# Performance work log

Hardware: AMD Instinct MI355X
Metric: run time of the kernel (lower is better)

The kernel has to match this reference:

```python
import jax, jax.numpy as jnp
import numpy as np

K_STEPS = 12
NUM_NEG = 10
B, C, T = 2, 512, 4096


def setup_inputs() -> dict:
    key = jax.random.key(0)
    k0, k1, k2, k3, k4 = jax.random.split(key, 5)
    feat_enc = jax.random.normal(k0, (B, C, T), dtype=jnp.float32)
    feat_context = jax.random.normal(k1, (B, C, T), dtype=jnp.float32)
    W = jax.random.normal(k2, (C, C), dtype=jnp.float32) / np.float32(np.sqrt(C))
    b = jax.random.normal(k3, (C,), dtype=jnp.float32) * 0.01
    # stands in for torch.multinomial draws inside the k-loop: one [T, num_neg]
    # index set per step (values in [0, T))
    neg_idx = jax.random.randint(k4, (K_STEPS, T, NUM_NEG), 0, T, dtype=jnp.int32)
    return {"feat_enc": feat_enc, "feat_context": feat_context, "W": W, "b": b,
            "neg_idx": neg_idx}


def reference(feat_enc, feat_context, W, b, neg_idx):
    # linear over channel dim: (transpose -> Linear -> transpose) == einsum
    c = jnp.einsum('bct,dc->bdt', feat_context, W) + b[None, :, None]  # [B,C,T]
    # cont[b,t,s] = sum_c z[b,c,t] * c[b,c,s]  -> [B,T,T]
    cont = jnp.einsum('bct,bcs->bts', feat_enc, c)
    Bn, Tlen, _ = cont.shape
    total = jnp.zeros((), dtype=cont.dtype)
    for k in range(K_STEPS):
        # positives: diagonal offset=-k -> cont[b, i+k, i], length T-k
        pos = jnp.diagonal(cont, offset=-k, axis1=1, axis2=2)
        pos_loss = jnp.sum(jax.nn.log_sigmoid(pos))
        # torch: neg[b, s, r] = cont[b, s, neg_idx[k, r, s]] for s<num_neg
        idx = neg_idx[k].T  # [num_neg, T]
        idx_b = jnp.broadcast_to(idx[None], (Bn, NUM_NEG, Tlen))
        neg = jnp.take_along_axis(cont[:, :NUM_NEG, :], idx_b, axis=2)
        neg_loss = jnp.sum(jax.nn.log_sigmoid(-neg))
        total = total + pos_loss + NUM_NEG * neg_loss
    return total
```

## Files before the change

### kernel.cpp

```cpp
#include <hip/hip_runtime.h>
#include <hip/hip_bf16.h>

constexpr int KST  = 12;
constexpr int NN   = 10;
constexpr int B    = 2;
constexpr int C    = 512;
constexpr int T    = 4096;
constexpr int BAND = 12;

typedef float f32x4  __attribute__((ext_vector_type(4)));
typedef short bf16x8 __attribute__((ext_vector_type(8)));

__device__ __forceinline__ float logsig(float x) {
    return fminf(x, 0.0f) - log1pf(expf(-fabsf(x)));
}
__device__ __forceinline__ unsigned short f2bf(float f) {
    union { float f; unsigned u; } v; v.f = f;
    unsigned r = v.u + 0x7fff + ((v.u >> 16) & 1);
    return (unsigned short)(r >> 16);
}

__global__ __launch_bounds__(256) void cast_w(
    const float* __restrict__ W, unsigned short* __restrict__ Wh)
{
    const int i = (blockIdx.x * 256 + threadIdx.x) * 4;
    const float4 v = *(const float4*)&W[i];
    short4 o;
    o.x = (short)f2bf(v.x);
    o.y = (short)f2bf(v.y);
    o.z = (short)f2bf(v.z);
    o.w = (short)f2bf(v.w);
    *(short4*)&Wh[i] = o;
}

__global__ __launch_bounds__(512) void fused_kernel(
    const unsigned short* __restrict__ Wh, const float* __restrict__ FC,
    const float* __restrict__ enc, const float* __restrict__ bias,
    float* __restrict__ negls, float* __restrict__ out)
{
    const int b  = blockIdx.y;
    const int n0 = blockIdx.x * 32;

    __shared__ unsigned short Bs[2][32][40];
    __shared__ unsigned short c_t[32 * 512];
    __shared__ unsigned short A_t[64 * 512];
    __shared__ float posred[8];

    const int tid  = threadIdx.x;
    const int lane = tid & 63;
    const int w    = tid >> 6;
    const int l15  = lane & 15;
    const int l4   = lane >> 4;
    const int mw   = w * 64;

    const int skk = tid >> 4;
    const int snn = (tid & 15) * 2;

    const float* FCb  = FC  + (size_t)b * C * T;
    const float* encb = enc + (size_t)b * C * T;

    f32x4 acc[4][2] = {};
    const unsigned short* Abase = Wh + (size_t)(mw + l15) * C + 8 * l4;

    float2 v = *(const float2*)&FCb[(size_t)skk * T + n0 + snn];
    bf16x8 afr[4];
    #pragma unroll
    for (int i = 0; i < 4; ++i) afr[i] = *(const bf16x8*)(Abase + i * 16 * C);

    Bs[0][snn][skk]     = f2bf(v.x);
    Bs[0][snn + 1][skk] = f2bf(v.y);

    int cur = 0;
    for (int ks = 0; ks < 16; ++ks) {
        __syncthreads();
        const int kn = (ks < 15) ? ks + 1 : 15;
        float2 vn = *(const float2*)&FCb[(size_t)(kn * 32 + skk) * T + n0 + snn];
        bf16x8 afn[4];
        #pragma unroll
        for (int i = 0; i < 4; ++i)
            afn[i] = *(const bf16x8*)(Abase + i * 16 * C + kn * 32);

        const bf16x8 bfr0 = *(const bf16x8*)&Bs[cur][l15][8 * l4];
        const bf16x8 bfr1 = *(const bf16x8*)&Bs[cur][16 + l15][8 * l4];

        #pragma unroll
        for (int i = 0; i < 4; ++i) {
            acc[i][0] = __builtin_amdgcn_mfma_f32_16x16x32_bf16(afr[i], bfr0, acc[i][0], 0, 0, 0);
            acc[i][1] = __builtin_amdgcn_mfma_f32_16x16x32_bf16(afr[i], bfr1, acc[i][1], 0, 0, 0);
        }
        Bs[cur ^ 1][snn][skk]     = f2bf(vn.x);
        Bs[cur ^ 1][snn + 1][skk] = f2bf(vn.y);
        #pragma unroll
        for (int i = 0; i < 4; ++i) afr[i] = afn[i];
        cur ^= 1;
    }

    #pragma unroll
    for (int i = 0; i < 4; ++i) {
        const int mb = mw + i * 16 + l4 * 4;
        const float4 bv = *(const float4*)&bias[mb];
        const int g = mb >> 3;
        #pragma unroll
        for (int j = 0; j < 2; ++j) {
            const int sp = j * 16 + l15;
            ushort4 u;
            u.x = f2bf(acc[i][j][0] + bv.x);
            u.y = f2bf(acc[i][j][1] + bv.y);
            u.z = f2bf(acc[i][j][2] + bv.z);
            u.w = f2bf(acc[i][j][3] + bv.w);
            const int off = sp * 1024 + ((g ^ (sp & 7)) << 4) + ((mb & 4) << 1);
            *(ushort4*)((char*)c_t + off) = u;
        }
    }

    {
        const bool safe = (n0 + 48 <= T);
        const int rr    = tid >> 3;
        const int cbase = (tid & 7) * 8;
        for (int dd = 0; dd < 8; ++dd) {
            const int d = dd * 64 + rr;
            float vals[8];
            if (cbase < 48) {
                if (safe) {
                    const float* p = encb + (size_t)d * T + n0 + cbase;
                    *(float4*)&vals[0] = *(const float4*)p;
                    *(float4*)&vals[4] = *(const float4*)(p + 4);
                } else {
                    #pragma unroll
                    for (int e = 0; e < 8; ++e) {
                        int t = n0 + cbase + e;
                        t = t < T ? t : T - 1;
                        vals[e] = encb[(size_t)d * T + t];
                    }
                }
            } else {
                const float* p = encb + (size_t)d * T + (cbase - 48);
                *(float4*)&vals[0] = *(const float4*)p;
                *(float4*)&vals[4] = *(const float4*)(p + 4);
            }
            const int gd = d >> 3;
            const int dl = (d & 7) << 1;
            #pragma unroll
            for (int e = 0; e < 8; ++e) {
                const int c = cbase + e;
                const int off = c * 1024 + ((gd ^ e) << 4) + dl;
                *(unsigned short*)((char*)A_t + off) = f2bf(vals[e]);
            }
        }
    }
    __syncthreads();

    const int i2 = w >> 1;
    const int j2 = w & 1;
    const int rg = i2 * 16 + l15;
    const int ci = (rg < 44) ? rg : ((rg < 54) ? rg + 4 : 63);
    const int sr = j2 * 16 + l15;
    const char* Abyte = (const char*)A_t + ci * 1024;
    const char* Bbyte = (const char*)c_t + sr * 1024;
    const int ax = ci & 7, bx = sr & 7;

    f32x4 dacc = {};
    #pragma unroll
    for (int ks = 0; ks < 16; ++ks) {
        const int ga = ks * 4 + l4;
        const bf16x8 a2 = *(const bf16x8*)(Abyte + ((ga ^ ax) << 4));
        const bf16x8 b2 = *(const bf16x8*)(Bbyte + ((ga ^ bx) << 4));
        dacc = __builtin_amdgcn_mfma_f32_16x16x32_bf16(a2, b2, dacc, 0, 0, 0);
    }

    float pos = 0.0f;
    const int colr = j2 * 16 + l15;
    const int scol = n0 + colr;
    #pragma unroll
    for (int r = 0; r < 4; ++r) {
        const int row = i2 * 16 + l4 * 4 + r;
        const float vv = dacc[r];
        if (row < 44) {
            const int k = row - colr;
            if (k >= 0 && k < BAND && scol + k < T) pos += logsig(vv);
        } else if (row < 54) {
            negls[((size_t)b * NN + (row - 44)) * T + scol] = logsig(-vv);
        }
    }
    #pragma unroll
    for (int off = 32; off > 0; off >>= 1) pos += __shfl_down(pos, off, 64);
    if (lane == 0) posred[w] = pos;
    __syncthreads();
    if (tid == 0) {
        float tsum = 0.0f;
        #pragma unroll
        for (int q = 0; q < 8; ++q) tsum += posred[q];
        atomicAdd(out, tsum);
    }
}

__global__ __launch_bounds__(256) void gather_kernel(
    const int4* __restrict__ nidx4, const float* __restrict__ negls,
    float* __restrict__ out)
{
    const int i4 = blockIdx.x * 256 + threadIdx.x;
    const int4 vv = nidx4[i4];
    const int base = i4 * 4;
    const int idxs[4] = {vv.x, vv.y, vv.z, vv.w};
    float local = 0.0f;
    #pragma unroll
    for (int e = 0; e < 4; ++e) {
        const int n = (base + e) % NN;
        local += negls[(size_t)n * T + idxs[e]]
               + negls[(size_t)(NN + n) * T + idxs[e]];
    }
    #pragma unroll
    for (int off = 32; off > 0; off >>= 1) local += __shfl_down(local, off, 64);
    __shared__ float wsum[4];
    if ((threadIdx.x & 63) == 0) wsum[threadIdx.x >> 6] = local;
    __syncthreads();
    if (threadIdx.x == 0)
        atomicAdd(out, (float)NN * (wsum[0] + wsum[1] + wsum[2] + wsum[3]));
}

extern "C" void kernel_launch(void* const* d_in, const int* in_sizes, int n_in,
                              void* d_out, int out_size, void* d_ws, size_t ws_size,
                              hipStream_t stream)
{
    const float* enc  = (const float*)d_in[0];
    const float* fc   = (const float*)d_in[1];
    const float* W    = (const float*)d_in[2];
    const float* bias = (const float*)d_in[3];
    const int*   nidx = (const int*)d_in[4];
    float* out = (float*)d_out;

    unsigned short* Wh = (unsigned short*)d_ws;
    float* negls = (float*)((char*)d_ws + (size_t)C * C * sizeof(unsigned short));

    hipMemsetAsync(out, 0, sizeof(float), stream);

    cast_w<<<C * C / (256 * 4), 256, 0, stream>>>(W, Wh);
    fused_kernel<<<dim3(T / 32, B), 512, 0, stream>>>(Wh, fc, enc, bias, negls, out);
    gather_kernel<<<KST * T * NN / (4 * 256), 256, 0, stream>>>(
        (const int4*)nidx, negls, out);
}
```

Baseline: 57.30 us.

## Stage full FC tile in LDS once, drop per-step syncs in projection GEMM

Replaces the double-buffered 32x32 FC staging loop (16 iterations each with a __syncthreads) with one up-front load in which each thread reads a full 32-wide row of FC and writes a swizzled bf16 tile covering all 512 channels. The projection GEMM then runs from LDS with no barriers in the K loop, and the result c is written back into the same LDS buffer, so the separate c_t array is removed. This is meant to cut barrier and latency overhead and to overlap the FC loads with the enc loads. In exchange, each thread issues wide loads of 32 floats, which raises register pressure, and the LDS stores use a scattered 2-byte pattern.

```diff
diff --git a/kernel.cpp b/kernel.cpp
--- a/kernel.cpp
+++ b/kernel.cpp
@@ -41,8 +41,7 @@
     const int b  = blockIdx.y;
     const int n0 = blockIdx.x * 32;
 
-    __shared__ unsigned short Bs[2][32][40];
-    __shared__ unsigned short c_t[32 * 512];
+    __shared__ unsigned short fc_t[32 * 512];
     __shared__ unsigned short A_t[64 * 512];
     __shared__ float posred[8];
 
@@ -53,63 +52,22 @@
     const int l4   = lane >> 4;
     const int mw   = w * 64;
 
-    const int skk = tid >> 4;
-    const int snn = (tid & 15) * 2;
-
     const float* FCb  = FC  + (size_t)b * C * T;
     const float* encb = enc + (size_t)b * C * T;
 
-    f32x4 acc[4][2] = {};
-    const unsigned short* Abase = Wh + (size_t)(mw + l15) * C + 8 * l4;
-
-    float2 v = *(const float2*)&FCb[(size_t)skk * T + n0 + snn];
-    bf16x8 afr[4];
-    #pragma unroll
-    for (int i = 0; i < 4; ++i) afr[i] = *(const bf16x8*)(Abase + i * 16 * C);
-
-    Bs[0][snn][skk]     = f2bf(v.x);
-    Bs[0][snn + 1][skk] = f2bf(v.y);
-
-    int cur = 0;
-    for (int ks = 0; ks < 16; ++ks) {
-        __syncthreads();
-        const int kn = (ks < 15) ? ks + 1 : 15;
-        float2 vn = *(const float2*)&FCb[(size_t)(kn * 32 + skk) * T + n0 + snn];
-        bf16x8 afn[4];
-        #pragma unroll
-        for (int i = 0; i < 4; ++i)
-            afn[i] = *(const bf16x8*)(Abase + i * 16 * C + kn * 32);
-
-        const bf16x8 bfr0 = *(const bf16x8*)&Bs[cur][l15][8 * l4];
-        const bf16x8 bfr1 = *(const bf16x8*)&Bs[cur][16 + l15][8 * l4];
-
-        #pragma unroll
-        for (int i = 0; i < 4; ++i) {
-            acc[i][0] = __builtin_amdgcn_mfma_f32_16x16x32_bf16(afr[i], bfr0, acc[i][0], 0, 0, 0);
-            acc[i][1] = __builtin_amdgcn_mfma_f32_16x16x32_bf16(afr[i], bfr1, acc[i][1], 0, 0, 0);
-        }
-        Bs[cur ^ 1][snn][skk]     = f2bf(vn.x);
-        Bs[cur ^ 1][snn + 1][skk] = f2bf(vn.y);
-        #pragma unroll
-        for (int i = 0; i < 4; ++i) afr[i] = afn[i];
-        cur ^= 1;
-    }
-
-    #pragma unroll
-    for (int i = 0; i < 4; ++i) {
-        const int mb = mw + i * 16 + l4 * 4;
-        const float4 bv = *(const float4*)&bias[mb];
-        const int g = mb >> 3;
-        #pragma unroll
-        for (int j = 0; j < 2; ++j) {
-            const int sp = j * 16 + l15;
-            ushort4 u;
-            u.x = f2bf(acc[i][j][0] + bv.x);
-            u.y = f2bf(acc[i][j][1] + bv.y);
-            u.z = f2bf(acc[i][j][2] + bv.z);
-            u.w = f2bf(acc[i][j][3] + bv.w);
-            const int off = sp * 1024 + ((g ^ (sp & 7)) << 4) + ((mb & 4) << 1);
-            *(ushort4*)((char*)c_t + off) = u;
+    {
+        const int k = tid;
+        const float* p = FCb + (size_t)k * T + n0;
+        float vals[32];
+        #pragma unroll
+        for (int q = 0; q < 8; ++q)
+            *(float4*)&vals[q * 4] = *(const float4*)(p + q * 4);
+        const int gk = k >> 3;
+        const int ke = (k & 7) * 2;
+        #pragma unroll
+        for (int j = 0; j < 32; ++j) {
+            const int off = j * 1024 + ((gk ^ (j & 7)) << 4) + ke;
+            *(unsigned short*)((char*)fc_t + off) = f2bf(vals[j]);
         }
     }
 
@@ -117,6 +75,7 @@
         const bool safe = (n0 + 48 <= T);
         const int rr    = tid >> 3;
         const int cbase = (tid & 7) * 8;
+        #pragma unroll
         for (int dd = 0; dd < 8; ++dd) {
             const int d = dd * 64 + rr;
             float vals[8];
@@ -150,21 +109,74 @@
     }
     __syncthreads();
 
+    f32x4 acc[4][2] = {};
+    const unsigned short* Abase = Wh + (size_t)(mw + l15) * C + 8 * l4;
+    const char* Bb0 = (const char*)fc_t + (size_t)l15 * 1024;
+    const char* Bb1 = (const char*)fc_t + (size_t)(16 + l15) * 1024;
+    const int bx = l15 & 7;
+
+    bf16x8 a_cur[4];
+    #pragma unroll
+    for (int i = 0; i < 4; ++i)
+        a_cur[i] = *(const bf16x8*)(Abase + (size_t)i * 16 * C);
+
+    #pragma unroll
+    for (int ks = 0; ks < 16; ++ks) {
+        bf16x8 a_nxt[4];
+        if (ks < 15) {
+            #pragma unroll
+            for (int i = 0; i < 4; ++i)
+                a_nxt[i] = *(const bf16x8*)(Abase + (size_t)i * 16 * C + (ks + 1) * 32);
+        }
+        const int ga = ks * 4 + l4;
+        const bf16x8 b0 = *(const bf16x8*)(Bb0 + ((ga ^ bx) << 4));
+        const bf16x8 b1 = *(const bf16x8*)(Bb1 + ((ga ^ bx) << 4));
+        #pragma unroll
+        for (int i = 0; i < 4; ++i) {
+            acc[i][0] = __builtin_amdgcn_mfma_f32_16x16x32_bf16(a_cur[i], b0, acc[i][0], 0, 0, 0);
+            acc[i][1] = __builtin_amdgcn_mfma_f32_16x16x32_bf16(a_cur[i], b1, acc[i][1], 0, 0, 0);
+        }
+        if (ks < 15) {
+            #pragma unroll
+            for (int i = 0; i < 4; ++i) a_cur[i] = a_nxt[i];
+        }
+    }
+    __syncthreads();
+
+    #pragma unroll
+    for (int i = 0; i < 4; ++i) {
+        const int mb = mw + i * 16 + l4 * 4;
+        const float4 bv = *(const float4*)&bias[mb];
+        const int g = mb >> 3;
+        #pragma unroll
+        for (int j = 0; j < 2; ++j) {
+            const int sp = j * 16 + l15;
+            ushort4 u;
+            u.x = f2bf(acc[i][j][0] + bv.x);
+            u.y = f2bf(acc[i][j][1] + bv.y);
+            u.z = f2bf(acc[i][j][2] + bv.z);
+            u.w = f2bf(acc[i][j][3] + bv.w);
+            const int off = sp * 1024 + ((g ^ (sp & 7)) << 4) + ((mb & 4) << 1);
+            *(ushort4*)((char*)fc_t + off) = u;
+        }
+    }
+    __syncthreads();
+
     const int i2 = w >> 1;
     const int j2 = w & 1;
     const int rg = i2 * 16 + l15;
     const int ci = (rg < 44) ? rg : ((rg < 54) ? rg + 4 : 63);
     const int sr = j2 * 16 + l15;
     const char* Abyte = (const char*)A_t + ci * 1024;
-    const char* Bbyte = (const char*)c_t + sr * 1024;
-    const int ax = ci & 7, bx = sr & 7;
+    const char* Bbyte = (const char*)fc_t + sr * 1024;
+    const int ax = ci & 7, bx2 = sr & 7;
 
     f32x4 dacc = {};
     #pragma unroll
     for (int ks = 0; ks < 16; ++ks) {
         const int ga = ks * 4 + l4;
         const bf16x8 a2 = *(const bf16x8*)(Abyte + ((ga ^ ax) << 4));
-        const bf16x8 b2 = *(const bf16x8*)(Bbyte + ((ga ^ bx) << 4));
+        const bf16x8 b2 = *(const bf16x8*)(Bbyte + ((ga ^ bx2) << 4));
         dacc = __builtin_amdgcn_mfma_f32_16x16x32_bf16(a2, b2, dacc, 0, 0, 0);
     }
 
```

After: 58.70 us. +2.4%, slower.

## Pre-transpose inputs to bf16 T-major layout and read MFMA operands from global

Applied to the files above, without the earlier changes.

Adds a prep kernel that transposes and casts both fc and enc from [B,C,T] fp32 into [B,T,C] bf16 workspace buffers. The fused kernel then loads MFMA fragments for both GEMMs directly from global memory, dropping the shared-memory staging of the B operand, the per-step barriers, and the scattered enc transpose into LDS. This removes in-kernel transposition work and LDS traffic, at the cost of an extra kernel launch and a full extra read and write of both inputs through the workspace.

```diff
diff --git a/kernel.cpp b/kernel.cpp
--- a/kernel.cpp
+++ b/kernel.cpp
@@ -10,6 +10,7 @@
 
 typedef float f32x4  __attribute__((ext_vector_type(4)));
 typedef short bf16x8 __attribute__((ext_vector_type(8)));
+typedef unsigned short u16x8 __attribute__((ext_vector_type(8)));
 
 __device__ __forceinline__ float logsig(float x) {
     return fminf(x, 0.0f) - log1pf(expf(-fabsf(x)));
@@ -33,17 +34,53 @@
     *(short4*)&Wh[i] = o;
 }
 
+__global__ __launch_bounds__(256) void prep_transpose(
+    const float* __restrict__ fc, const float* __restrict__ enc,
+    unsigned short* __restrict__ fcT, unsigned short* __restrict__ encT)
+{
+    const int z  = blockIdx.z;
+    const float* src = (z < 2 ? fc : enc) + (size_t)(z & 1) * C * T;
+    unsigned short* dst = (z < 2 ? fcT : encT) + (size_t)(z & 1) * T * C;
+    const int t0 = blockIdx.x * 64;
+    const int c0 = blockIdx.y * 64;
+
+    __shared__ float lt[64][65];
+
+    const int tid = threadIdx.x;
+    const int tq = (tid & 15) * 4;
+    const int cr = tid >> 4;
+    #pragma unroll
+    for (int p = 0; p < 4; ++p) {
+        const int c_row = p * 16 + cr;
+        const float4 v = *(const float4*)&src[(size_t)(c0 + c_row) * T + t0 + tq];
+        lt[tq + 0][c_row] = v.x;
+        lt[tq + 1][c_row] = v.y;
+        lt[tq + 2][c_row] = v.z;
+        lt[tq + 3][c_row] = v.w;
+    }
+    __syncthreads();
+
+    const int t_row = tid >> 2;
+    const int cq    = (tid & 3) * 16;
+    u16x8 o0, o1;
+    #pragma unroll
+    for (int u = 0; u < 8; ++u) o0[u] = f2bf(lt[t_row][cq + u]);
+    #pragma unroll
+    for (int u = 0; u < 8; ++u) o1[u] = f2bf(lt[t_row][cq + 8 + u]);
+    unsigned short* dp = dst + (size_t)(t0 + t_row) * C + c0 + cq;
+    *(u16x8*)dp       = o0;
+    *(u16x8*)(dp + 8) = o1;
+}
+
 __global__ __launch_bounds__(512) void fused_kernel(
-    const unsigned short* __restrict__ Wh, const float* __restrict__ FC,
-    const float* __restrict__ enc, const float* __restrict__ bias,
+    const unsigned short* __restrict__ Wh, const unsigned short* __restrict__ fcT,
+    const unsigned short* __restrict__ encT, const float* __restrict__ bias,
     float* __restrict__ negls, float* __restrict__ out)
 {
     const int b  = blockIdx.y;
     const int n0 = blockIdx.x * 32;
 
-    __shared__ unsigned short Bs[2][32][40];
     __shared__ unsigned short c_t[32 * 512];
-    __shared__ unsigned short A_t[64 * 512];
     __shared__ float posred[8];
 
     const int tid  = threadIdx.x;
@@ -53,46 +90,25 @@
     const int l4   = lane >> 4;
     const int mw   = w * 64;
 
-    const int skk = tid >> 4;
-    const int snn = (tid & 15) * 2;
-
-    const float* FCb  = FC  + (size_t)b * C * T;
-    const float* encb = enc + (size_t)b * C * T;
+    const unsigned short* fcTb  = fcT  + (size_t)b * T * C;
+    const unsigned short* encTb = encT + (size_t)b * T * C;
 
     f32x4 acc[4][2] = {};
-    const unsigned short* Abase = Wh + (size_t)(mw + l15) * C + 8 * l4;
-
-    float2 v = *(const float2*)&FCb[(size_t)skk * T + n0 + snn];
-    bf16x8 afr[4];
-    #pragma unroll
-    for (int i = 0; i < 4; ++i) afr[i] = *(const bf16x8*)(Abase + i * 16 * C);
-
-    Bs[0][snn][skk]     = f2bf(v.x);
-    Bs[0][snn + 1][skk] = f2bf(v.y);
-
-    int cur = 0;
+    const unsigned short* Ab  = Wh   + (size_t)(mw + l15) * C + l4 * 8;
+    const unsigned short* Bb0 = fcTb + (size_t)(n0 + l15) * C + l4 * 8;
+    const unsigned short* Bb1 = Bb0 + 16 * C;
+
+    #pragma unroll 4
     for (int ks = 0; ks < 16; ++ks) {
-        __syncthreads();
-        const int kn = (ks < 15) ? ks + 1 : 15;
-        float2 vn = *(const float2*)&FCb[(size_t)(kn * 32 + skk) * T + n0 + snn];
-        bf16x8 afn[4];
-        #pragma unroll
-        for (int i = 0; i < 4; ++i)
-            afn[i] = *(const bf16x8*)(Abase + i * 16 * C + kn * 32);
-
-        const bf16x8 bfr0 = *(const bf16x8*)&Bs[cur][l15][8 * l4];
-        const bf16x8 bfr1 = *(const bf16x8*)&Bs[cur][16 + l15][8 * l4];
-
+        const int ko = ks * 32;
+        const bf16x8 b0 = *(const bf16x8*)(Bb0 + ko);
+        const bf16x8 b1 = *(const bf16x8*)(Bb1 + ko);
         #pragma unroll
         for (int i = 0; i < 4; ++i) {
-            acc[i][0] = __builtin_amdgcn_mfma_f32_16x16x32_bf16(afr[i], bfr0, acc[i][0], 0, 0, 0);
-            acc[i][1] = __builtin_amdgcn_mfma_f32_16x16x32_bf16(afr[i], bfr1, acc[i][1], 0, 0, 0);
+            const bf16x8 a = *(const bf16x8*)(Ab + (size_t)i * 16 * C + ko);
+            acc[i][0] = __builtin_amdgcn_mfma_f32_16x16x32_bf16(a, b0, acc[i][0], 0, 0, 0);
+            acc[i][1] = __builtin_amdgcn_mfma_f32_16x16x32_bf16(a, b1, acc[i][1], 0, 0, 0);
         }
-        Bs[cur ^ 1][snn][skk]     = f2bf(vn.x);
-        Bs[cur ^ 1][snn + 1][skk] = f2bf(vn.y);
-        #pragma unroll
-        for (int i = 0; i < 4; ++i) afr[i] = afn[i];
-        cur ^= 1;
     }
 
     #pragma unroll
@@ -112,59 +128,25 @@
             *(ushort4*)((char*)c_t + off) = u;
         }
     }
-
-    {
-        const bool safe = (n0 + 48 <= T);
-        const int rr    = tid >> 3;
-        const int cbase = (tid & 7) * 8;
-        for (int dd = 0; dd < 8; ++dd) {
-            const int d = dd * 64 + rr;
-            float vals[8];
-            if (cbase < 48) {
-                if (safe) {
-                    const float* p = encb + (size_t)d * T + n0 + cbase;
-                    *(float4*)&vals[0] = *(const float4*)p;
-                    *(float4*)&vals[4] = *(const float4*)(p + 4);
-                } else {
-                    #pragma unroll
-                    for (int e = 0; e < 8; ++e) {
-                        int t = n0 + cbase + e;
-                        t = t < T ? t : T - 1;
-                        vals[e] = encb[(size_t)d * T + t];
-                    }
-                }
-            } else {
-                const float* p = encb + (size_t)d * T + (cbase - 48);
-                *(float4*)&vals[0] = *(const float4*)p;
-                *(float4*)&vals[4] = *(const float4*)(p + 4);
-            }
-            const int gd = d >> 3;
-            const int dl = (d & 7) << 1;
-            #pragma unroll
-            for (int e = 0; e < 8; ++e) {
-                const int c = cbase + e;
-                const int off = c * 1024 + ((gd ^ e) << 4) + dl;
-                *(unsigned short*)((char*)A_t + off) = f2bf(vals[e]);
-            }
-        }
-    }
     __syncthreads();
 
     const int i2 = w >> 1;
     const int j2 = w & 1;
     const int rg = i2 * 16 + l15;
-    const int ci = (rg < 44) ? rg : ((rg < 54) ? rg + 4 : 63);
-    const int sr = j2 * 16 + l15;
-    const char* Abyte = (const char*)A_t + ci * 1024;
-    const char* Bbyte = (const char*)c_t + sr * 1024;
-    const int ax = ci & 7, bx = sr & 7;
+    int ti;
+    if (rg < 44) { ti = n0 + rg; ti = ti < T ? ti : T - 1; }
+    else if (rg < 54) ti = rg - 44;
+    else ti = 0;
+    const unsigned short* A2p = encTb + (size_t)ti * C + l4 * 8;
+    const char* B2b = (const char*)c_t + (j2 * 16 + l15) * 1024;
+    const int bx2 = l15 & 7;
 
     f32x4 dacc = {};
-    #pragma unroll
+    #pragma unroll 4
     for (int ks = 0; ks < 16; ++ks) {
+        const bf16x8 a2 = *(const bf16x8*)(A2p + ks * 32);
         const int ga = ks * 4 + l4;
-        const bf16x8 a2 = *(const bf16x8*)(Abyte + ((ga ^ ax) << 4));
-        const bf16x8 b2 = *(const bf16x8*)(Bbyte + ((ga ^ bx) << 4));
+        const bf16x8 b2 = *(const bf16x8*)(B2b + ((ga ^ bx2) << 4));
         dacc = __builtin_amdgcn_mfma_f32_16x16x32_bf16(a2, b2, dacc, 0, 0, 0);
     }
 
@@ -229,13 +211,16 @@
     const int*   nidx = (const int*)d_in[4];
     float* out = (float*)d_out;
 
-    unsigned short* Wh = (unsigned short*)d_ws;
-    float* negls = (float*)((char*)d_ws + (size_t)C * C * sizeof(unsigned short));
+    unsigned short* fcT  = (unsigned short*)d_ws;
+    unsigned short* encT = fcT + (size_t)B * T * C;
+    unsigned short* Wh   = encT + (size_t)B * T * C;
+    float* negls = (float*)(Wh + (size_t)C * C);
 
     hipMemsetAsync(out, 0, sizeof(float), stream);
 
     cast_w<<<C * C / (256 * 4), 256, 0, stream>>>(W, Wh);
-    fused_kernel<<<dim3(T / 32, B), 512, 0, stream>>>(Wh, fc, enc, bias, negls, out);
+    prep_transpose<<<dim3(T / 64, C / 64, 4), 256, 0, stream>>>(fc, enc, fcT, encT);
+    fused_kernel<<<dim3(T / 32, B), 512, 0, stream>>>(Wh, fcT, encT, bias, negls, out);
     gather_kernel<<<KST * T * NN / (4 * 256), 256, 0, stream>>>(
         (const int4*)nidx, negls, out);
 }
```

After: 64.54 us. 12.6% more time.
